# Kernel optimization log

Measured on AMD Instinct MI355X. Metric: run time of the kernel, lower is better.

## Reference

```python
import jax, jax.numpy as jnp
import numpy as np

B, S_IMG, S_TXT, S_BOK = 1, 2048, 512, 4
DM, H, DH, R = 3072, 24, 128, 16
LORA_SCALE, LORA_ALPHA, BOKEH_SCALE = 1.0, 16.0, 1.0
EPS = 1e-6


def _rms_norm(x, w):
    # normalize over head_dim (last axis), Flux RMSNorm eps=1e-6
    var = jnp.mean(jnp.square(x), axis=-1, keepdims=True)
    return x * jax.lax.rsqrt(var + EPS) * w


def _lora(x, w_down, w_up):
    # LoRALinear: up(down(x)) * alpha/rank
    return (x @ w_down.T) @ w_up.T * (LORA_ALPHA / R)


def _apply_rope(x, cos, sin):
    # x: [B,H,S,D]; cos/sin: [S,D]; diffusers use_real=True, unbind_dim=-1 (interleaved pairs)
    x1 = x[..., 0::2]
    x2 = x[..., 1::2]
    rot = jnp.stack([-x2, x1], axis=-1).reshape(x.shape)
    return x * cos[None, None] + rot * sin[None, None]


def _sdpa(q, k, v):
    # q:[B,H,Sq,D] k,v:[B,H,Sk,D]
    scale = 1.0 / jnp.sqrt(jnp.asarray(q.shape[-1], q.dtype))
    scores = jnp.einsum('bhqd,bhkd->bhqk', q, k) * scale
    p = jax.nn.softmax(scores, axis=-1)
    return jnp.einsum('bhqk,bhkd->bhqd', p, v)


def setup_inputs() -> dict:
    key = jax.random.key(0)
    ks = jax.random.split(key, 40)
    std = 0.02
    d = {}
    d['hidden_states'] = jax.random.normal(ks[0], (B, S_IMG, DM), jnp.float32)
    d['encoder_hidden_states'] = jax.random.normal(ks[1], (B, S_TXT, DM), jnp.float32)
    d['bokeh_embeds'] = jax.random.normal(ks[2], (B, S_BOK, DM), jnp.float32)
    theta = jax.random.uniform(ks[3], (S_TXT + S_IMG, DH // 2), jnp.float32) * 2 * np.pi
    theta = jnp.repeat(theta, 2, axis=-1)  # interleaved pairs share angle
    d['rope_cos'] = jnp.cos(theta)
    d['rope_sin'] = jnp.sin(theta)
    # base attention params
    for i, nm in enumerate(['Wq', 'Wk', 'Wv', 'Waq', 'Wak', 'Wav', 'Wo', 'Wao']):
        d[nm] = jax.random.normal(ks[4 + i], (DM, DM), jnp.float32) * std
    for i, nm in enumerate(['bq', 'bk', 'bv', 'baq', 'bak', 'bav', 'bo', 'bao']):
        d[nm] = jax.random.normal(ks[12 + i], (DM,), jnp.float32) * std
    for i, nm in enumerate(['norm_q_w', 'norm_k_w', 'norm_aq_w', 'norm_ak_w']):
        d[nm] = 1.0 + jax.random.normal(ks[20 + i], (DH,), jnp.float32) * std
    # LoRA adapters (up weights random, not zero, for nontrivial math)
    for i, nm in enumerate(['kb_down', 'vb_down', 'qadp_down', 'kadp_down']):
        d[nm] = jax.random.normal(ks[24 + i], (R, DM), jnp.float32) * (1.0 / R)
    for i, nm in enumerate(['kb_up', 'vb_up', 'qadp_up', 'kadp_up']):
        d[nm] = jax.random.normal(ks[28 + i], (DM, R), jnp.float32) * std
    return d


def reference(hidden_states, encoder_hidden_states, bokeh_embeds, rope_cos, rope_sin,
              Wq, Wk, Wv, Waq, Wak, Wav, Wo, Wao,
              bq, bk, bv, baq, bak, bav, bo, bao,
              norm_q_w, norm_k_w, norm_aq_w, norm_ak_w,
              kb_down, vb_down, qadp_down, kadp_down,
              kb_up, vb_up, qadp_up, kadp_up):
    Bsz = encoder_hidden_states.shape[0]

    def heads(x):  # [B,S,DM] -> [B,H,S,DH]
        return x.reshape(Bsz, -1, H, DH).transpose(0, 2, 1, 3)

    q = hidden_states @ Wq.T + bq
    k = hidden_states @ Wk.T + bk
    v = hidden_states @ Wv.T + bv
    q = q + LORA_SCALE * _lora(q, qadp_down, qadp_up)
    k = k + LORA_SCALE * _lora(k, kadp_down, kadp_up)
    q, k, v = heads(q), heads(k), heads(v)
    q = _rms_norm(q, norm_q_w)
    k = _rms_norm(k, norm_k_w)

    eq = heads(encoder_hidden_states @ Waq.T + baq)
    ek = heads(encoder_hidden_states @ Wak.T + bak)
    ev = heads(encoder_hidden_states @ Wav.T + bav)
    eq = _rms_norm(eq, norm_aq_w)
    ek = _rms_norm(ek, norm_ak_w)

    q = jnp.concatenate([eq, q], axis=2)
    k = jnp.concatenate([ek, k], axis=2)
    v = jnp.concatenate([ev, v], axis=2)

    q = _apply_rope(q, rope_cos, rope_sin)
    k = _apply_rope(k, rope_cos, rope_sin)

    out = _sdpa(q, k, v)  # [B,H,S,DH]
    out = out.transpose(0, 2, 1, 3).reshape(Bsz, -1, H * DH)

    # bokeh pass
    kd = heads(_lora(bokeh_embeds, kb_down, kb_up))
    vd = heads(_lora(bokeh_embeds, vb_down, vb_up))
    cam = _sdpa(q, kd, vd).transpose(0, 2, 1, 3).reshape(Bsz, -1, H * DH)
    out = out + BOKEH_SCALE * cam

    enc_out = out[:, :S_TXT]
    img_out = out[:, S_TXT:]
    img_out = img_out @ Wo.T + bo
    enc_out = enc_out @ Wao.T + bao
    return (img_out, enc_out)
```

## Files before the change

kernel.cpp:

```cpp
#include <hip/hip_runtime.h>

#define DMDL 3072
#define SEQ  2560
#define STXT 512
#define HEADS 24
#define DHD  128
#define WB9 9437184

typedef float f32x4 __attribute__((ext_vector_type(4)));
typedef __bf16 bf16x8 __attribute__((ext_vector_type(8)));
typedef unsigned short u16x4 __attribute__((ext_vector_type(4)));

static __device__ __forceinline__ unsigned short f2bf(float f) {
  unsigned u = __float_as_uint(f);
  u += 0x7fffu + ((u >> 16) & 1u);
  return (unsigned short)(u >> 16);
}

static __device__ __forceinline__ float fexp2(float x) {
  return __builtin_amdgcn_exp2f(x);
}

static __device__ __forceinline__ void gload16(const unsigned short* g, unsigned short* l) {
  __builtin_amdgcn_global_load_lds(
      (const __attribute__((address_space(1))) unsigned int*)g,
      (__attribute__((address_space(3))) unsigned int*)l, 16, 0, 0);
}

__global__ __launch_bounds__(256) void convf2b_kernel(
    const float* __restrict__ src, unsigned short* __restrict__ dst) {
  const int idx4 = blockIdx.x * 256 + threadIdx.x;
  float4 v = *(const float4*)(src + (size_t)idx4 * 4);
  u16x4 b = { f2bf(v.x), f2bf(v.y), f2bf(v.z), f2bf(v.w) };
  *(u16x4*)(dst + (size_t)idx4 * 4) = b;
}

__global__ __launch_bounds__(256) void convw_kernel(
    const float* __restrict__ s0, const float* __restrict__ s1,
    const float* __restrict__ s2, unsigned short* __restrict__ dst) {
  const float* src = (blockIdx.y == 0) ? s0 : (blockIdx.y == 1) ? s1 : s2;
  const size_t idx4 = (size_t)blockIdx.x * 256 + threadIdx.x;
  float4 v = *(const float4*)(src + idx4 * 4);
  u16x4 b = { f2bf(v.x), f2bf(v.y), f2bf(v.z), f2bf(v.w) };
  *(u16x4*)(dst + (size_t)blockIdx.y * WB9 + idx4 * 4) = b;
}

__device__ __forceinline__ void gemm_body(
    const unsigned short* __restrict__ A, const unsigned short* __restrict__ Bw,
    const float* __restrict__ bias, float* __restrict__ C,
    int row0, int col0) {
  __shared__ unsigned short Al[2][128][64];
  __shared__ unsigned short Bl[2][128][64];
  const int t = threadIdx.x, w = t >> 6, l = t & 63;
  const int wr = (w >> 1) << 6, wc = (w & 1) << 6;
  const int l15 = l & 15, lg = l >> 4;
  f32x4 acc[4][4];
#pragma unroll
  for (int i = 0; i < 4; i++)
#pragma unroll
    for (int j = 0; j < 4; j++) acc[i][j] = (f32x4){0.f, 0.f, 0.f, 0.f};

#define GSTAGE(buf, kt)                                                       \
  {                                                                           \
    const int kk = (kt) << 6;                                                 \
    _Pragma("unroll")                                                         \
    for (int g = 0; g < 4; g++) {                                             \
      const int jb = ((w << 2) + g) << 6;                                     \
      const int jl = jb + l;                                                  \
      const int row = jl >> 3, sl = jl & 7;                                   \
      const int col = ((sl ^ (row & 7)) << 3);                                \
      gload16(A  + (size_t)(row0 + row) * DMDL + kk + col,                    \
              &Al[buf][0][0] + (size_t)jb * 8);                               \
      gload16(Bw + (size_t)(col0 + row) * DMDL + kk + col,                    \
              &Bl[buf][0][0] + (size_t)jb * 8);                               \
    }                                                                         \
  }

  GSTAGE(0, 0)
  GSTAGE(1, 1)
  asm volatile("s_waitcnt vmcnt(8)" ::: "memory");
  __syncthreads();

  const int NT = DMDL >> 6;
  for (int kt = 0; kt < NT; kt++) {
    const int b = kt & 1;
#pragma unroll
    for (int kf = 0; kf < 2; kf++) {
      bf16x8 af[4], bfr[4];
#pragma unroll
      for (int i = 0; i < 4; i++) {
        const int ra = wr + (i << 4) + l15;
        af[i]  = *(const bf16x8*)&Al[b][ra][(((kf << 2) + lg) ^ (ra & 7)) << 3];
        const int rb = wc + (i << 4) + l15;
        bfr[i] = *(const bf16x8*)&Bl[b][rb][(((kf << 2) + lg) ^ (rb & 7)) << 3];
      }
      __builtin_amdgcn_s_setprio(1);
#pragma unroll
      for (int i = 0; i < 4; i++)
#pragma unroll
        for (int j = 0; j < 4; j++)
          acc[i][j] = __builtin_amdgcn_mfma_f32_16x16x32_bf16(af[i], bfr[j], acc[i][j], 0, 0, 0);
      __builtin_amdgcn_s_setprio(0);
    }
    __syncthreads();
    if (kt + 2 < NT) {
      GSTAGE(b, kt + 2)
      asm volatile("s_waitcnt vmcnt(8)" ::: "memory");
    } else {
      asm volatile("s_waitcnt vmcnt(0)" ::: "memory");
    }
    __syncthreads();
  }
#undef GSTAGE

#pragma unroll
  for (int i = 0; i < 4; i++)
#pragma unroll
    for (int j = 0; j < 4; j++) {
      const int col = col0 + wc + (j << 4) + l15;
      const float bb = bias[col];
      const int rbase = row0 + wr + (i << 4) + (lg << 2);
#pragma unroll
      for (int r2 = 0; r2 < 4; r2++)
        C[(size_t)(rbase + r2) * DMDL + col] = acc[i][j][r2] + bb;
    }
}

__global__ __launch_bounds__(256) void gemm3_kernel(
    const unsigned short* __restrict__ A, const unsigned short* __restrict__ w3,
    const float* __restrict__ b0, const float* __restrict__ b1, const float* __restrict__ b2,
    float* __restrict__ c0, float* __restrict__ c1, float* __restrict__ c2, int M) {
  const int nM = M >> 7;
  const int nwg = nM * 72;
  const int cpx = nwg >> 3;
  const int sid = (blockIdx.x & 7) * cpx + (blockIdx.x >> 3);
  const int bxx = sid / nM, by = sid - bxx * nM;
  const int grp = bxx / 24, bx = bxx - grp * 24;
  const unsigned short* Bw = w3 + (size_t)grp * WB9;
  const float* bias = (grp == 0) ? b0 : (grp == 1) ? b1 : b2;
  float* C = (grp == 0) ? c0 : (grp == 1) ? c1 : c2;
  gemm_body(A, Bw, bias, C, by << 7, bx << 7);
}

__global__ __launch_bounds__(256) void gemm_out_kernel(
    const unsigned short* __restrict__ attnbf, const unsigned short* __restrict__ w3,
    const float* __restrict__ bo, const float* __restrict__ bao,
    float* __restrict__ out) {
  const int sid = (blockIdx.x & 7) * 60 + (blockIdx.x >> 3);
  if (sid < 384) {
    const int bx = sid >> 4, by = sid & 15;
    gemm_body(attnbf + (size_t)STXT * DMDL, w3, bo, out, by << 7, bx << 7);
  } else {
    const int s2 = sid - 384;
    const int bx = s2 >> 2, by = s2 & 3;
    gemm_body(attnbf, w3 + WB9, bao, out + (size_t)2048 * DMDL, by << 7, bx << 7);
  }
}

__global__ __launch_bounds__(256) void lora_down2_kernel(
    const float* __restrict__ q0, const float* __restrict__ k0,
    const float* __restrict__ qad, const float* __restrict__ kad,
    float* __restrict__ tmpq, float* __restrict__ tmpk) {
  const int t = threadIdx.x, w = t >> 6, l = t & 63;
  const int m = blockIdx.x;
  const float* X = blockIdx.y ? k0 : q0;
  const float* dwn = blockIdx.y ? kad : qad;
  float* tmp = blockIdx.y ? tmpk : tmpq;
  const float* x = X + (size_t)m * DMDL;
  float acc[16];
#pragma unroll
  for (int r = 0; r < 16; r++) acc[r] = 0.f;
  for (int k = t; k < DMDL; k += 256) {
    float xv = x[k];
#pragma unroll
    for (int r = 0; r < 16; r++) acc[r] += xv * dwn[r * DMDL + k];
  }
#pragma unroll
  for (int off = 1; off < 64; off <<= 1)
#pragma unroll
    for (int r = 0; r < 16; r++) acc[r] += __shfl_xor(acc[r], off);
  __shared__ float red[4][16];
  if (l == 0)
#pragma unroll
    for (int r = 0; r < 16; r++) red[w][r] = acc[r];
  __syncthreads();
  if (t < 16) tmp[(size_t)m * 16 + t] = red[0][t] + red[1][t] + red[2][t] + red[3][t];
}

#define QSCALE 0.12751743f
__global__ __launch_bounds__(256) void pack_kernel(
    const float* __restrict__ q0, const float* __restrict__ k0,
    const float* __restrict__ eq, const float* __restrict__ ek,
    const float* __restrict__ tmpq, const float* __restrict__ tmpk,
    const float* __restrict__ qau, const float* __restrict__ kau,
    const float* __restrict__ nq, const float* __restrict__ nk,
    const float* __restrict__ naq, const float* __restrict__ nak,
    const float* __restrict__ rc, const float* __restrict__ rsn,
    unsigned short* __restrict__ Qp, unsigned short* __restrict__ Kp) {
  const int t = threadIdx.x, w = t >> 6, l = t & 63;
  const int s = blockIdx.x * 4 + w;
  const int h = blockIdx.y;
  const int which = blockIdx.z;
  const int n = h * DHD + 2 * l;
  float2 x;
  const float* nw;
  if (s < STXT) {
    x = *(const float2*)(((which == 0) ? eq : ek) + (size_t)s * DMDL + n);
    nw = (which == 0) ? naq : nak;
  } else {
    x = *(const float2*)(((which == 0) ? q0 : k0) + (size_t)(s - STXT) * DMDL + n);
    nw = (which == 0) ? nq : nk;
    const float* tv = ((which == 0) ? tmpq : tmpk) + (size_t)(s - STXT) * 16;
    const float* uv = ((which == 0) ? qau : kau) + (size_t)n * 16;
    float l1 = 0.f, l2 = 0.f;
#pragma unroll
    for (int r = 0; r < 16; r++) { l1 += tv[r] * uv[r]; l2 += tv[r] * uv[16 + r]; }
    x.x += l1; x.y += l2;
  }
  float ss = x.x * x.x + x.y * x.y;
#pragma unroll
  for (int off = 1; off < 64; off <<= 1) ss += __shfl_xor(ss, off);
  float inv = rsqrtf(ss * (1.f / 128.f) + 1e-6f);
  float xw1 = x.x * inv * nw[2 * l];
  float xw2 = x.y * inv * nw[2 * l + 1];
  float c1 = rc[(size_t)s * DHD + 2 * l], c2 = rc[(size_t)s * DHD + 2 * l + 1];
  float s1 = rsn[(size_t)s * DHD + 2 * l], s2 = rsn[(size_t)s * DHD + 2 * l + 1];
  float y1 = xw1 * c1 - xw2 * s1;
  float y2 = xw2 * c2 + xw1 * s2;
  if (which == 0) { y1 *= QSCALE; y2 *= QSCALE; }
  unsigned short* dst = ((which == 0) ? Qp : Kp) + ((size_t)h * SEQ + s) * DHD + 2 * l;
  unsigned pk = (unsigned)f2bf(y1) | ((unsigned)f2bf(y2) << 16);
  *(unsigned*)dst = pk;
}

__global__ __launch_bounds__(256) void vpackT_kernel(
    const float* __restrict__ v0, const float* __restrict__ ev,
    unsigned short* __restrict__ Vtg) {
  __shared__ unsigned short tile[64][136];
  const int t = threadIdx.x;
  const int s0 = blockIdx.x << 6;
  const int h = blockIdx.y;
  const float* src;
  int srow;
  if (s0 < STXT) { src = ev; srow = s0; } else { src = v0; srow = s0 - STXT; }
#pragma unroll
  for (int p = 0; p < 8; p++) {
    int idx4 = (p << 8) + t;
    int r = idx4 >> 5, c4 = idx4 & 31;
    float4 v = *(const float4*)(src + (size_t)(srow + r) * DMDL + h * DHD + (c4 << 2));
    u16x4 b = { f2bf(v.x), f2bf(v.y), f2bf(v.z), f2bf(v.w) };
    *(u16x4*)&tile[r][c4 << 2] = b;
  }
  __syncthreads();
  const int d = t >> 1, sc = (t & 1) << 5;
  unsigned short outv[32];
#pragma unroll
  for (int e = 0; e < 32; e++) outv[e] = tile[sc + e][d];
  unsigned short* dst = Vtg + ((size_t)h * DHD + d) * SEQ + s0 + sc;
#pragma unroll
  for (int q = 0; q < 4; q++)
    *(uint4*)(dst + (q << 3)) = *(uint4*)&outv[q << 3];
}

__global__ __launch_bounds__(256) void bokeh_down_kernel(
    const float* __restrict__ bok, const float* __restrict__ kbd,
    const float* __restrict__ vbd, float* __restrict__ tkv) {
  const int t = threadIdx.x, w = t >> 6, l = t & 63;
  const int mat = blockIdx.x >> 2, j = blockIdx.x & 3;
  const float* dwn = mat ? vbd : kbd;
  const float* x = bok + (size_t)j * DMDL;
  float acc[16];
#pragma unroll
  for (int r = 0; r < 16; r++) acc[r] = 0.f;
  for (int k = t; k < DMDL; k += 256) {
    float xv = x[k];
#pragma unroll
    for (int r = 0; r < 16; r++) acc[r] += xv * dwn[r * DMDL + k];
  }
#pragma unroll
  for (int off = 1; off < 64; off <<= 1)
#pragma unroll
    for (int r = 0; r < 16; r++) acc[r] += __shfl_xor(acc[r], off);
  __shared__ float red[4][16];
  if (l == 0)
#pragma unroll
    for (int r = 0; r < 16; r++) red[w][r] = acc[r];
  __syncthreads();
  if (t < 16) tkv[(mat * 4 + j) * 16 + t] = red[0][t] + red[1][t] + red[2][t] + red[3][t];
}

__global__ __launch_bounds__(256) void bokeh_up_kernel(
    const float* __restrict__ tkv, const float* __restrict__ kbu,
    const float* __restrict__ vbu, float* __restrict__ kdvd) {
  const int idx = blockIdx.x * 256 + threadIdx.x;
  const int mat = idx / 12288, rem = idx % 12288;
  const int j = rem / DMDL, n = rem % DMDL;
  const float* up = mat ? vbu : kbu;
  const float* tv = tkv + (mat * 4 + j) * 16;
  float s = 0.f;
#pragma unroll
  for (int r = 0; r < 16; r++) s += tv[r] * up[(size_t)n * 16 + r];
  kdvd[(size_t)(mat * 4 + j) * DMDL + n] = s;
}

__global__ __launch_bounds__(256) void attn_kernel(
    const unsigned short* __restrict__ Qp, const unsigned short* __restrict__ Kp,
    const unsigned short* __restrict__ Vtg, const float* __restrict__ kdvd,
    unsigned short* __restrict__ attnbf) {
  __shared__ unsigned short Klds[128][128];
  __shared__ unsigned short Vt[128][128];
  __shared__ unsigned short Pl[4][2048];
  const int t = threadIdx.x, w = t >> 6, l = t & 63;
  const int l15 = l & 15, lg = l >> 4;
  const int h = blockIdx.y;
  const int q0r = blockIdx.x * 64;
  const unsigned short* Qh = Qp + (size_t)h * SEQ * DHD;
  const unsigned short* Kh = Kp + (size_t)h * SEQ * DHD;
  const unsigned short* Vh = Vtg + (size_t)h * DHD * SEQ;
  char* Pw = (char*)&Pl[w][0];

  bf16x8 qf[4];
  {
    const unsigned short* qsrc = Qh + (size_t)(q0r + w * 16 + l15) * DHD + (lg << 3);
#pragma unroll
    for (int kf = 0; kf < 4; kf++) qf[kf] = *(const bf16x8*)(qsrc + kf * 32);
  }
  f32x4 o[8];
#pragma unroll
  for (int nc = 0; nc < 8; nc++) o[nc] = (f32x4){0.f, 0.f, 0.f, 0.f};
  float m = -1e30f, sum = 0.f;

  for (int kv0 = 0; kv0 < SEQ; kv0 += 128) {
    __syncthreads();
#pragma unroll
    for (int g = 0; g < 8; g++) {
      const int jb = ((g << 2) + w) << 6;
      const int jl = jb + l;
      const int row = jl >> 4, sl = jl & 15;
      const int col = (sl ^ (row & 7)) << 3;
      gload16(Kh + (size_t)(kv0 + row) * DHD + col, ((unsigned short*)Klds) + (size_t)jb * 8);
      gload16(Vh + (size_t)row * SEQ + kv0 + col, ((unsigned short*)Vt) + (size_t)jb * 8);
    }
    asm volatile("s_waitcnt vmcnt(0)" ::: "memory");
    __syncthreads();
    f32x4 sacc[8];
    __builtin_amdgcn_s_setprio(1);
#pragma unroll
    for (int c = 0; c < 8; c++) {
      sacc[c] = (f32x4){0.f, 0.f, 0.f, 0.f};
      const int krow = c * 16 + l15;
#pragma unroll
      for (int kf = 0; kf < 4; kf++) {
        bf16x8 kb = *(const bf16x8*)&Klds[krow][(((kf << 2) + lg) ^ (krow & 7)) << 3];
        sacc[c] = __builtin_amdgcn_mfma_f32_16x16x32_bf16(kb, qf[kf], sacc[c], 0, 0, 0);
      }
    }
    __builtin_amdgcn_s_setprio(0);
    float cm[8];
#pragma unroll
    for (int c = 0; c < 8; c++)
      cm[c] = fmaxf(fmaxf(sacc[c][0], sacc[c][1]), fmaxf(sacc[c][2], sacc[c][3]));
    float pmax = fmaxf(fmaxf(fmaxf(cm[0], cm[1]), fmaxf(cm[2], cm[3])),
                       fmaxf(fmaxf(cm[4], cm[5]), fmaxf(cm[6], cm[7])));
    pmax = fmaxf(pmax, __shfl_xor(pmax, 16));
    pmax = fmaxf(pmax, __shfl_xor(pmax, 32));
    const bool skip = __all(pmax <= m + 8.f);
    const float mnew = skip ? m : fmaxf(m, pmax);
    float ps = 0.f;
#pragma unroll
    for (int c = 0; c < 8; c++) {
      float p0 = fexp2(sacc[c][0] - mnew);
      float p1 = fexp2(sacc[c][1] - mnew);
      float p2 = fexp2(sacc[c][2] - mnew);
      float p3 = fexp2(sacc[c][3] - mnew);
      ps += (p0 + p1) + (p2 + p3);
      unsigned lo, hi;
      asm("v_cvt_pk_bf16_f32 %0, %1, %2" : "=v"(lo) : "v"(p0), "v"(p1));
      asm("v_cvt_pk_bf16_f32 %0, %1, %2" : "=v"(hi) : "v"(p2), "v"(p3));
      const int byteoff = (l15 << 8) + (((((c << 1) + (lg >> 1)) ^ (l15 & 7))) << 4) + ((lg & 1) << 3);
      *(uint2*)(Pw + byteoff) = make_uint2(lo, hi);
    }
    ps += __shfl_xor(ps, 16);
    ps += __shfl_xor(ps, 32);
    if (!skip) {
      const float sc = fexp2(m - mnew);
      sum = sum * sc + ps;
      m = mnew;
      float s0 = __shfl(sc, (lg << 2) + 0);
      float s1 = __shfl(sc, (lg << 2) + 1);
      float s2 = __shfl(sc, (lg << 2) + 2);
      float s3 = __shfl(sc, (lg << 2) + 3);
#pragma unroll
      for (int nc = 0; nc < 8; nc++) {
        o[nc][0] *= s0; o[nc][1] *= s1; o[nc][2] *= s2; o[nc][3] *= s3;
      }
    } else {
      sum += ps;
    }
    __builtin_amdgcn_s_setprio(1);
#pragma unroll
    for (int kf2 = 0; kf2 < 4; kf2++) {
      bf16x8 pa = *(const bf16x8*)(Pw + (l15 << 8) + ((((kf2 << 2) + lg) ^ (l15 & 7)) << 4));
#pragma unroll
      for (int nc = 0; nc < 8; nc++) {
        const int vrow = nc * 16 + l15;
        bf16x8 vb = *(const bf16x8*)&Vt[vrow][(((kf2 << 2) + lg) ^ (vrow & 7)) << 3];
        o[nc] = __builtin_amdgcn_mfma_f32_16x16x32_bf16(pa, vb, o[nc], 0, 0, 0);
      }
    }
    __builtin_amdgcn_s_setprio(0);
  }

  float rinv[4];
  {
    float su0 = __shfl(sum, (lg << 2) + 0);
    float su1 = __shfl(sum, (lg << 2) + 1);
    float su2 = __shfl(sum, (lg << 2) + 2);
    float su3 = __shfl(sum, (lg << 2) + 3);
    rinv[0] = 1.f / su0; rinv[1] = 1.f / su1; rinv[2] = 1.f / su2; rinv[3] = 1.f / su3;
  }

  __syncthreads();
  float* kdl = (float*)&Klds[0][0];
  {
    const int j8 = t >> 5, d4 = (t & 31) << 2;
    *(float4*)&kdl[j8 * 128 + d4] = *(const float4*)(kdvd + (size_t)j8 * DMDL + h * DHD + d4);
  }
  __syncthreads();
  float q32[4][8];
#pragma unroll
  for (int kf = 0; kf < 4; kf++)
#pragma unroll
    for (int r = 0; r < 8; r++) q32[kf][r] = (float)qf[kf][r];
  float pj[4];
#pragma unroll
  for (int jb = 0; jb < 4; jb++) {
    float d = 0.f;
#pragma unroll
    for (int kf = 0; kf < 4; kf++)
#pragma unroll
      for (int r = 0; r < 8; r++)
        d += q32[kf][r] * kdl[jb * 128 + (kf << 5) + (lg << 3) + r];
    d += __shfl_xor(d, 16);
    d += __shfl_xor(d, 32);
    pj[jb] = d;
  }
  float cmx = fmaxf(fmaxf(pj[0], pj[1]), fmaxf(pj[2], pj[3]));
  float cs = 0.f;
#pragma unroll
  for (int jb = 0; jb < 4; jb++) { pj[jb] = fexp2(pj[jb] - cmx); cs += pj[jb]; }
  float ci = 1.f / cs;
#pragma unroll
  for (int jb = 0; jb < 4; jb++) pj[jb] *= ci;
  float* pnl = kdl + 1024 + (w << 6);
  if (lg == 0) {
#pragma unroll
    for (int jb = 0; jb < 4; jb++) pnl[l15 * 4 + jb] = pj[jb];
  }
  __syncthreads();
  float pr[4][4];
#pragma unroll
  for (int j = 0; j < 4; j++)
#pragma unroll
    for (int jb = 0; jb < 4; jb++) pr[j][jb] = pnl[(((lg << 2) + j) << 2) + jb];
  const float* vdl = kdl + 512;
#pragma unroll
  for (int nc = 0; nc < 8; nc++) {
    const int col = (nc << 4) + l15;
#pragma unroll
    for (int j = 0; j < 4; j++) {
      float cam = pr[j][0] * vdl[col] + pr[j][1] * vdl[128 + col] +
                  pr[j][2] * vdl[256 + col] + pr[j][3] * vdl[384 + col];
      float outv = o[nc][j] * rinv[j] + cam;
      const int row = q0r + (w << 4) + (lg << 2) + j;
      attnbf[(size_t)row * DMDL + h * DHD + col] = f2bf(outv);
    }
  }
}

extern "C" void kernel_launch(void* const* d_in, const int* in_sizes, int n_in,
                              void* d_out, int out_size, void* d_ws, size_t ws_size,
                              hipStream_t stream) {
  (void)in_sizes; (void)n_in; (void)out_size; (void)ws_size;
  const float* hs  = (const float*)d_in[0];
  const float* enc = (const float*)d_in[1];
  const float* bok = (const float*)d_in[2];
  const float* rc  = (const float*)d_in[3];
  const float* rsn = (const float*)d_in[4];
  const float* Wq  = (const float*)d_in[5];
  const float* Wk  = (const float*)d_in[6];
  const float* Wv  = (const float*)d_in[7];
  const float* Waq = (const float*)d_in[8];
  const float* Wak = (const float*)d_in[9];
  const float* Wav = (const float*)d_in[10];
  const float* Wo  = (const float*)d_in[11];
  const float* Wao = (const float*)d_in[12];
  const float* bq  = (const float*)d_in[13];
  const float* bk  = (const float*)d_in[14];
  const float* bv  = (const float*)d_in[15];
  const float* baq = (const float*)d_in[16];
  const float* bak = (const float*)d_in[17];
  const float* bav = (const float*)d_in[18];
  const float* bo  = (const float*)d_in[19];
  const float* bao = (const float*)d_in[20];
  const float* nq  = (const float*)d_in[21];
  const float* nk  = (const float*)d_in[22];
  const float* naq = (const float*)d_in[23];
  const float* nak = (const float*)d_in[24];
  const float* kbd = (const float*)d_in[25];
  const float* vbd = (const float*)d_in[26];
  const float* qad = (const float*)d_in[27];
  const float* kad = (const float*)d_in[28];
  const float* kbu = (const float*)d_in[29];
  const float* vbu = (const float*)d_in[30];
  const float* qau = (const float*)d_in[31];
  const float* kau = (const float*)d_in[32];

  char* ws = (char*)d_ws;
  unsigned short* w3     = (unsigned short*)(ws + 0);
  unsigned short* hs_bf  = (unsigned short*)(ws + 56623104);
  unsigned short* enc_bf = (unsigned short*)(ws + 69206016);
  float* q0   = (float*)(ws + 72351744);
  float* k0   = (float*)(ws + 97517568);
  float* v0   = (float*)(ws + 122683392);
  float* eq   = (float*)(ws + 147849216);
  float* ek   = (float*)(ws + 154140672);
  float* ev   = (float*)(ws + 160432128);
  float* tmpq = (float*)(ws + 166723584);
  float* tmpk = (float*)(ws + 166854656);
  float* tkv  = (float*)(ws + 166985728);
  float* kdvd = (float*)(ws + 166986240);
  unsigned short* Qp  = (unsigned short*)(ws + 167084544);
  unsigned short* Kp  = (unsigned short*)(ws + 182813184);
  unsigned short* Vtg = (unsigned short*)(ws + 72351744);
  unsigned short* attnbf = (unsigned short*)(ws + 122683392);

  float* out = (float*)d_out;

  dim3 blk(256);

  convf2b_kernel<<<6144, blk, 0, stream>>>(hs, hs_bf);
  convf2b_kernel<<<1536, blk, 0, stream>>>(enc, enc_bf);
  bokeh_down_kernel<<<8, blk, 0, stream>>>(bok, kbd, vbd, tkv);
  bokeh_up_kernel<<<96, blk, 0, stream>>>(tkv, kbu, vbu, kdvd);

  convw_kernel<<<dim3(9216, 3), blk, 0, stream>>>(Wq, Wk, Wv, w3);
  gemm3_kernel<<<1152, blk, 0, stream>>>(hs_bf, w3, bq, bk, bv, q0, k0, v0, 2048);
  convw_kernel<<<dim3(9216, 3), blk, 0, stream>>>(Waq, Wak, Wav, w3);
  gemm3_kernel<<<288, blk, 0, stream>>>(enc_bf, w3, baq, bak, bav, eq, ek, ev, 512);

  lora_down2_kernel<<<dim3(2048, 2), blk, 0, stream>>>(q0, k0, qad, kad, tmpq, tmpk);

  pack_kernel<<<dim3(SEQ / 4, HEADS, 2), blk, 0, stream>>>(
      q0, k0, eq, ek, tmpq, tmpk, qau, kau, nq, nk, naq, nak, rc, rsn, Qp, Kp);
  vpackT_kernel<<<dim3(SEQ / 64, HEADS), blk, 0, stream>>>(v0, ev, Vtg);

  attn_kernel<<<dim3(SEQ / 64, HEADS), blk, 0, stream>>>(Qp, Kp, Vtg, kdvd, attnbf);

  convw_kernel<<<dim3(9216, 2), blk, 0, stream>>>(Wo, Wao, Wao, w3);
  gemm_out_kernel<<<480, blk, 0, stream>>>(attnbf, w3, bo, bao, out);
}
```

Baseline: 728.2 us.

## Shrink GEMM K-tile to 32 with repacked swizzled LDS layout

```diff
diff --git a/kernel.cpp b/kernel.cpp
--- a/kernel.cpp
+++ b/kernel.cpp
@@ -49,8 +49,8 @@
     const unsigned short* __restrict__ A, const unsigned short* __restrict__ Bw,
     const float* __restrict__ bias, float* __restrict__ C,
     int row0, int col0) {
-  __shared__ unsigned short Al[2][128][64];
-  __shared__ unsigned short Bl[2][128][64];
+  __shared__ unsigned short Al[2][64][64];
+  __shared__ unsigned short Bl[2][64][64];
   const int t = threadIdx.x, w = t >> 6, l = t & 63;
   const int wr = (w >> 1) << 6, wc = (w & 1) << 6;
   const int l15 = l & 15, lg = l >> 4;
@@ -62,54 +62,54 @@
 
 #define GSTAGE(buf, kt)                                                       \
   {                                                                           \
-    const int kk = (kt) << 6;                                                 \
+    const int kk = (kt) << 5;                                                 \
     _Pragma("unroll")                                                         \
-    for (int g = 0; g < 4; g++) {                                             \
-      const int jb = ((w << 2) + g) << 6;                                     \
-      const int jl = jb + l;                                                  \
-      const int row = jl >> 3, sl = jl & 7;                                   \
-      const int col = ((sl ^ (row & 7)) << 3);                                \
-      gload16(A  + (size_t)(row0 + row) * DMDL + kk + col,                    \
-              &Al[buf][0][0] + (size_t)jb * 8);                               \
-      gload16(Bw + (size_t)(col0 + row) * DMDL + kk + col,                    \
-              &Bl[buf][0][0] + (size_t)jb * 8);                               \
+    for (int r = 0; r < 2; r++) {                                             \
+      const int jb = ((r << 2) + w) << 10;                                    \
+      const int o = jb + (l << 4);                                            \
+      const int lrow = o >> 7, phys = (o >> 4) & 7;                           \
+      const int slot = phys ^ (lrow & 7);                                     \
+      const int grow = (lrow << 1) + (slot >> 2);                             \
+      const int gcol = (slot & 3) << 3;                                       \
+      gload16(A  + (size_t)(row0 + grow) * DMDL + kk + gcol,                  \
+              (unsigned short*)&Al[buf][0][0] + (jb >> 1));                   \
+      gload16(Bw + (size_t)(col0 + grow) * DMDL + kk + gcol,                  \
+              (unsigned short*)&Bl[buf][0][0] + (jb >> 1));                   \
     }                                                                         \
   }
 
   GSTAGE(0, 0)
   GSTAGE(1, 1)
-  asm volatile("s_waitcnt vmcnt(8)" ::: "memory");
-  __syncthreads();
-
-  const int NT = DMDL >> 6;
+
+  const int NT = DMDL >> 5;
   for (int kt = 0; kt < NT; kt++) {
     const int b = kt & 1;
-#pragma unroll
-    for (int kf = 0; kf < 2; kf++) {
-      bf16x8 af[4], bfr[4];
-#pragma unroll
-      for (int i = 0; i < 4; i++) {
-        const int ra = wr + (i << 4) + l15;
-        af[i]  = *(const bf16x8*)&Al[b][ra][(((kf << 2) + lg) ^ (ra & 7)) << 3];
-        const int rb = wc + (i << 4) + l15;
-        bfr[i] = *(const bf16x8*)&Bl[b][rb][(((kf << 2) + lg) ^ (rb & 7)) << 3];
-      }
-      __builtin_amdgcn_s_setprio(1);
-#pragma unroll
-      for (int i = 0; i < 4; i++)
-#pragma unroll
-        for (int j = 0; j < 4; j++)
-          acc[i][j] = __builtin_amdgcn_mfma_f32_16x16x32_bf16(af[i], bfr[j], acc[i][j], 0, 0, 0);
-      __builtin_amdgcn_s_setprio(0);
-    }
+    if (kt + 1 < NT)
+      asm volatile("s_waitcnt vmcnt(4)" ::: "memory");
+    else
+      asm volatile("s_waitcnt vmcnt(0)" ::: "memory");
     __syncthreads();
-    if (kt + 2 < NT) {
-      GSTAGE(b, kt + 2)
-      asm volatile("s_waitcnt vmcnt(8)" ::: "memory");
-    } else {
-      asm volatile("s_waitcnt vmcnt(0)" ::: "memory");
-    }
+    bf16x8 af[4], bfr[4];
+#pragma unroll
+    for (int i = 0; i < 4; i++) {
+      const int ra = wr + (i << 4) + l15;
+      const int pa = ra >> 1;
+      const int sa = (((ra & 1) << 2) + lg) ^ (pa & 7);
+      af[i] = *(const bf16x8*)&Al[b][pa][sa << 3];
+      const int rb = wc + (i << 4) + l15;
+      const int pb = rb >> 1;
+      const int sb = (((rb & 1) << 2) + lg) ^ (pb & 7);
+      bfr[i] = *(const bf16x8*)&Bl[b][pb][sb << 3];
+    }
+    __builtin_amdgcn_s_setprio(1);
+#pragma unroll
+    for (int i = 0; i < 4; i++)
+#pragma unroll
+      for (int j = 0; j < 4; j++)
+        acc[i][j] = __builtin_amdgcn_mfma_f32_16x16x32_bf16(af[i], bfr[j], acc[i][j], 0, 0, 0);
+    __builtin_amdgcn_s_setprio(0);
     __syncthreads();
+    if (kt + 2 < NT) GSTAGE(b, kt + 2)
   }
 #undef GSTAGE
 
```

Result: faster. 690.4 us (-5.2%).
